# Kernel tuning notes

Hardware: AMD Instinct MI355X
Metric: run time of the kernel (lower is better)

## Reference

```python
import jax, jax.numpy as jnp
import numpy as np

EPS = 1e-5

def _layernorm(x, g, b):
    m = jnp.mean(x, axis=-1, keepdims=True)
    v = jnp.mean((x - m) ** 2, axis=-1, keepdims=True)
    return (x - m) * jax.lax.rsqrt(v + EPS) * g + b

def _mish(x):
    return x * jnp.tanh(jax.nn.softplus(x))

def setup_inputs() -> dict:
    key = jax.random.key(0)
    ks = jax.random.split(key, 6)
    N, D, Hd, P = 768, 256, 256, 128
    return {
        "h_fused": jax.random.normal(ks[0], (N, D), jnp.float32),
        "W0": jax.random.normal(ks[1], (D, Hd), jnp.float32) / np.sqrt(D),
        "b0": jnp.zeros((Hd,), jnp.float32),
        "g0": jnp.ones((Hd,), jnp.float32),
        "be0": jnp.zeros((Hd,), jnp.float32),
        "W1": jax.random.normal(ks[2], (Hd, P), jnp.float32) / np.sqrt(Hd),
        "b1": jnp.zeros((P,), jnp.float32),
        "Wc1": jax.random.normal(ks[3], (2 * P, Hd), jnp.float32) / np.sqrt(2 * P),
        "bc1": jnp.zeros((Hd,), jnp.float32),
        "gc": jnp.ones((Hd,), jnp.float32),
        "bec": jnp.zeros((Hd,), jnp.float32),
        "Wc2": jax.random.normal(ks[4], (Hd, 1), jnp.float32) / np.sqrt(Hd),
        "bc2": jnp.zeros((1,), jnp.float32),
    }

def reference(h_fused, W0, b0, g0, be0, W1, b1, Wc1, bc1, gc, bec, Wc2, bc2):
    # pre_proj: Linear -> LayerNorm -> Mish -> (Dropout p=0) -> Linear
    H = _mish(_layernorm(h_fused @ W0 + b0, g0, be0)) @ W1 + b1  # [N, P]
    P = H.shape[-1]
    # classifier Linear on concat(h_i, h_j): split weight rows so the
    # [N,N,2P] concat tensor is never materialized (identical math).
    Wi, Wj = Wc1[:P], Wc1[P:]
    fi = H @ Wi  # [N, Hd]
    fj = H @ Wj  # [N, Hd]
    pair = fi[:, None, :] + fj[None, :, :] + bc1  # [N, N, Hd]
    h = _mish(_layernorm(pair, gc, bec))
    logits = (h @ Wc2 + bc2)[..., 0]  # [N, N]
    logits = logits[None]  # B=1 (batch_ptr=None path)
    N = logits.shape[-1]
    matrix_mask = jnp.ones((1, N, N), dtype=bool)
    return (logits, matrix_mask)
```

## Files before the change

kernel.cpp:

```cpp
#include <hip/hip_runtime.h>

#define EPS 1e-5f
#define LOGITS_N (768 * 768)
#define LOG2E 1.4426950408889634f
#define LN2   0.6931471805599453f

__device__ __forceinline__ float mishf(float z) {
    float t = __expf(fminf(z, 40.f));
    float u = t * (t + 2.f);
    return z * u * __builtin_amdgcn_rcpf(u + 2.f);
}

__device__ __forceinline__ float block_sum(float v, float* red) {
#pragma unroll
    for (int off = 32; off > 0; off >>= 1) v += __shfl_down(v, off, 64);
    const int lane = threadIdx.x & 63, wid = threadIdx.x >> 6;
    __syncthreads();
    if (lane == 0) red[wid] = v;
    __syncthreads();
    return red[0] + red[1] + red[2] + red[3];
}

__global__ __launch_bounds__(256) void k1_rows(
    const float* __restrict__ h, const float* __restrict__ W0,
    const float* __restrict__ b0, const float* __restrict__ g0,
    const float* __restrict__ be0, const float* __restrict__ W1,
    const float* __restrict__ b1, const float* __restrict__ Wc1,
    const float* __restrict__ bc1, const float* __restrict__ gc,
    const float* __restrict__ bec, const float* __restrict__ wc2,
    float* __restrict__ fi, float* __restrict__ fjb,
    float* __restrict__ stats, float* __restrict__ Gp,
    float* __restrict__ Ep, float* __restrict__ Wp) {
    __shared__ float shi[256][2];
    __shared__ float sai[256][2];
    __shared__ float sHi[128][2];
    __shared__ float red[4];
    __shared__ float part[4][64][12];
    const int t = threadIdx.x;
    const int i0 = blockIdx.x * 2;
    if (blockIdx.x == 0) {
        Gp[t] = gc[t] * LOG2E;
        Ep[t] = bec[t] * LOG2E;
        Wp[t] = wc2[t] * LN2;
    }
    shi[t][0] = h[i0 * 256 + t];
    shi[t][1] = h[i0 * 256 + 256 + t];
    __syncthreads();
    {
        const int kc = t >> 6, jg = t & 63;
        const float* w0p = W0 + (kc * 64) * 256 + jg * 4;
        float ax[2][4] = {};
#pragma unroll 8
        for (int kk = 0; kk < 64; ++kk) {
            float4 w = *(const float4*)(w0p + kk * 256);
            float2 hh = *(const float2*)&shi[kc * 64 + kk][0];
            ax[0][0] = fmaf(hh.x, w.x, ax[0][0]);
            ax[0][1] = fmaf(hh.x, w.y, ax[0][1]);
            ax[0][2] = fmaf(hh.x, w.z, ax[0][2]);
            ax[0][3] = fmaf(hh.x, w.w, ax[0][3]);
            ax[1][0] = fmaf(hh.y, w.x, ax[1][0]);
            ax[1][1] = fmaf(hh.y, w.y, ax[1][1]);
            ax[1][2] = fmaf(hh.y, w.z, ax[1][2]);
            ax[1][3] = fmaf(hh.y, w.w, ax[1][3]);
        }
        float* pp = &part[kc][jg][0];
#pragma unroll
        for (int c = 0; c < 4; ++c) { pp[c * 2] = ax[0][c]; pp[c * 2 + 1] = ax[1][c]; }
    }
    __syncthreads();
    float x0, x1;
    {
        const int m = t >> 2, c = t & 3;
        x0 = b0[t]; x1 = x0;
#pragma unroll
        for (int kc = 0; kc < 4; ++kc) {
            x0 += part[kc][m][c * 2 + 0];
            x1 += part[kc][m][c * 2 + 1];
        }
    }
    {
        float s1 = block_sum(x0, red), s2 = block_sum(x0 * x0, red);
        float mean = s1 * (1.f / 256.f);
        float var = fmaxf(s2 * (1.f / 256.f) - mean * mean, 0.f);
        float rs = __builtin_amdgcn_rsqf(var + EPS);
        sai[t][0] = mishf((x0 - mean) * rs * g0[t] + be0[t]);
        s1 = block_sum(x1, red); s2 = block_sum(x1 * x1, red);
        mean = s1 * (1.f / 256.f);
        var = fmaxf(s2 * (1.f / 256.f) - mean * mean, 0.f);
        rs = __builtin_amdgcn_rsqf(var + EPS);
        sai[t][1] = mishf((x1 - mean) * rs * g0[t] + be0[t]);
    }
    __syncthreads();
    {
        const int kc = t >> 5, jg = t & 31;
        const float* w1p = W1 + (kc * 32) * 128 + jg * 4;
        float ah[2][4] = {};
#pragma unroll 8
        for (int kk = 0; kk < 32; ++kk) {
            float4 w = *(const float4*)(w1p + kk * 128);
            float2 ss = *(const float2*)&sai[kc * 32 + kk][0];
            ah[0][0] = fmaf(ss.x, w.x, ah[0][0]);
            ah[0][1] = fmaf(ss.x, w.y, ah[0][1]);
            ah[0][2] = fmaf(ss.x, w.z, ah[0][2]);
            ah[0][3] = fmaf(ss.x, w.w, ah[0][3]);
            ah[1][0] = fmaf(ss.y, w.x, ah[1][0]);
            ah[1][1] = fmaf(ss.y, w.y, ah[1][1]);
            ah[1][2] = fmaf(ss.y, w.z, ah[1][2]);
            ah[1][3] = fmaf(ss.y, w.w, ah[1][3]);
        }
        float* pp = &part[0][0][0] + (kc * 32 + jg) * 12;
#pragma unroll
        for (int c = 0; c < 4; ++c) { pp[c * 2] = ah[0][c]; pp[c * 2 + 1] = ah[1][c]; }
    }
    __syncthreads();
    {
        const int r = t >> 7, jj = t & 127;
        float hv = b1[jj];
        const float* pf = &part[0][0][0];
#pragma unroll
        for (int kc = 0; kc < 8; ++kc)
            hv += pf[(kc * 32 + (jj >> 2)) * 12 + (jj & 3) * 2 + r];
        sHi[jj][r] = hv;
    }
    __syncthreads();
    float avi[2][4] = {}, avj[2][4] = {};
    {
        const int kc = t >> 6, jg = t & 63;
        const float* wip = Wc1 + (kc * 32) * 256 + jg * 4;
        const float* wjp = Wc1 + (128 + kc * 32) * 256 + jg * 4;
#pragma unroll 4
        for (int kk = 0; kk < 32; ++kk) {
            float4 wa = *(const float4*)(wip + kk * 256);
            float4 wb = *(const float4*)(wjp + kk * 256);
            float2 hh = *(const float2*)&sHi[kc * 32 + kk][0];
            avi[0][0] = fmaf(hh.x, wa.x, avi[0][0]);
            avi[0][1] = fmaf(hh.x, wa.y, avi[0][1]);
            avi[0][2] = fmaf(hh.x, wa.z, avi[0][2]);
            avi[0][3] = fmaf(hh.x, wa.w, avi[0][3]);
            avi[1][0] = fmaf(hh.y, wa.x, avi[1][0]);
            avi[1][1] = fmaf(hh.y, wa.y, avi[1][1]);
            avi[1][2] = fmaf(hh.y, wa.z, avi[1][2]);
            avi[1][3] = fmaf(hh.y, wa.w, avi[1][3]);
            avj[0][0] = fmaf(hh.x, wb.x, avj[0][0]);
            avj[0][1] = fmaf(hh.x, wb.y, avj[0][1]);
            avj[0][2] = fmaf(hh.x, wb.z, avj[0][2]);
            avj[0][3] = fmaf(hh.x, wb.w, avj[0][3]);
            avj[1][0] = fmaf(hh.y, wb.x, avj[1][0]);
            avj[1][1] = fmaf(hh.y, wb.y, avj[1][1]);
            avj[1][2] = fmaf(hh.y, wb.z, avj[1][2]);
            avj[1][3] = fmaf(hh.y, wb.w, avj[1][3]);
        }
        float* pp = &part[kc][jg][0];
#pragma unroll
        for (int c = 0; c < 4; ++c) { pp[c * 2] = avi[0][c]; pp[c * 2 + 1] = avi[1][c]; }
    }
    __syncthreads();
    float vi0 = 0.f, vi1 = 0.f;
    {
        const int m = t >> 2, c = t & 3;
#pragma unroll
        for (int kc = 0; kc < 4; ++kc) {
            vi0 += part[kc][m][c * 2 + 0];
            vi1 += part[kc][m][c * 2 + 1];
        }
    }
    __syncthreads();
    {
        const int kc = t >> 6, jg = t & 63;
        float* pp = &part[kc][jg][0];
#pragma unroll
        for (int c = 0; c < 4; ++c) { pp[c * 2] = avj[0][c]; pp[c * 2 + 1] = avj[1][c]; }
    }
    __syncthreads();
    float vj0, vj1;
    {
        const int m = t >> 2, c = t & 3;
        vj0 = bc1[t]; vj1 = vj0;
#pragma unroll
        for (int kc = 0; kc < 4; ++kc) {
            vj0 += part[kc][m][c * 2 + 0];
            vj1 += part[kc][m][c * 2 + 1];
        }
    }
    fi[i0 * 256 + t] = vi0;
    fi[(i0 + 1) * 256 + t] = vi1;
    fjb[i0 * 256 + t] = vj0;
    fjb[(i0 + 1) * 256 + t] = vj1;
    {
        float su = block_sum(vi0, red), sq = block_sum(vi0 * vi0, red);
        float sv = block_sum(vj0, red), sw = block_sum(vj0 * vj0, red);
        if (t == 0) {
            stats[i0 * 4 + 0] = su * (1.f / 256.f);
            stats[i0 * 4 + 1] = sq * (1.f / 256.f);
            stats[i0 * 4 + 2] = sv * (1.f / 256.f);
            stats[i0 * 4 + 3] = sw * (1.f / 256.f);
        }
        su = block_sum(vi1, red); sq = block_sum(vi1 * vi1, red);
        sv = block_sum(vj1, red); sw = block_sum(vj1 * vj1, red);
        if (t == 0) {
            stats[(i0 + 1) * 4 + 0] = su * (1.f / 256.f);
            stats[(i0 + 1) * 4 + 1] = sq * (1.f / 256.f);
            stats[(i0 + 1) * 4 + 2] = sv * (1.f / 256.f);
            stats[(i0 + 1) * 4 + 3] = sw * (1.f / 256.f);
        }
    }
}

__global__ __launch_bounds__(256) void k3_pair(
    const float* __restrict__ fi, const float* __restrict__ fjb,
    const float* __restrict__ stats, const float* __restrict__ Gp,
    const float* __restrict__ Ep, const float* __restrict__ Wp,
    const float* __restrict__ bc2, float* __restrict__ out, int write_mask) {
    __shared__ float FI[16][260];
    __shared__ float FJ[16][260];
    __shared__ float Gs[256];
    const int tid = threadIdx.x;
    const int i0 = blockIdx.y * 16, j0 = blockIdx.x * 16;
#pragma unroll
    for (int l = 0; l < 4; ++l) {
        int idx = tid + l * 256;
        int r = idx >> 6, c = (idx & 63) * 4;
        *(float4*)&FI[r][c] = *(const float4*)&fi[(i0 + r) * 256 + c];
        *(float4*)&FJ[r][c] = *(const float4*)&fjb[(j0 + r) * 256 + c];
    }
    Gs[tid] = Gp[tid];
    const int ti = tid >> 4, tj = tid & 15;
    float a_i = stats[(i0 + ti) * 4 + 0];
    float s_i = stats[(i0 + ti) * 4 + 1];
    float b_j = stats[(j0 + tj) * 4 + 2];
    float t_j = stats[(j0 + tj) * 4 + 3];
    __syncthreads();
    const float* FIp = &FI[ti][0];
    const float* FJp = &FJ[tj][0];
    float dot[4] = {0.f, 0.f, 0.f, 0.f};
#pragma unroll 8
    for (int d4 = 0; d4 < 64; ++d4) {
        float4 xi = *(const float4*)&FIp[d4 * 4];
        float4 xj = *(const float4*)&FJp[d4 * 4];
        dot[0] = fmaf(xi.x, xj.x, dot[0]);
        dot[1] = fmaf(xi.y, xj.y, dot[1]);
        dot[2] = fmaf(xi.z, xj.z, dot[2]);
        dot[3] = fmaf(xi.w, xj.w, dot[3]);
    }
    float m = a_i + b_j;
    float ex2 = s_i + t_j + (dot[0] + dot[1] + dot[2] + dot[3]) * (2.f / 256.f);
    float var = fmaxf(ex2 - m * m, 0.f);
    float rs = __builtin_amdgcn_rsqf(var + EPS);
    float c0 = -m * rs;
    const float4* Ep4 = (const float4*)Ep;
    const float4* Wp4 = (const float4*)Wp;
    float acc[4] = {0.f, 0.f, 0.f, 0.f};
#pragma unroll 8
    for (int d4 = 0; d4 < 64; ++d4) {
        float4 xi = *(const float4*)&FIp[d4 * 4];
        float4 xj = *(const float4*)&FJp[d4 * 4];
        float4 g4 = *(const float4*)&Gs[d4 * 4];
        float4 e4 = Ep4[d4];
        float4 w4 = Wp4[d4];
        float gs[4] = {g4.x, g4.y, g4.z, g4.w};
        float es[4] = {e4.x, e4.y, e4.z, e4.w};
        float vs[4] = {w4.x, w4.y, w4.z, w4.w};
        float xs[4] = {xi.x + xj.x, xi.y + xj.y, xi.z + xj.z, xi.w + xj.w};
        float y[4], v[4];
#pragma unroll
        for (int c = 0; c < 4; ++c) {
            float p = fmaf(xs[c], rs, c0);
            y[c] = fmaf(p, gs[c], es[c]);
            float tt = __builtin_amdgcn_exp2f(y[c]);
            v[c] = fmaf(tt, tt + 2.f, 2.f);
        }
        float p01 = v[0] * v[1], p23 = v[2] * v[3];
        float rr = __builtin_amdgcn_rcpf(p01 * p23);
        float i01 = rr * p23, i23 = rr * p01;
        float inv[4] = {i01 * v[1], i01 * v[0], i23 * v[3], i23 * v[2]};
#pragma unroll
        for (int c = 0; c < 4; ++c) {
            float my = fmaf(y[c] * inv[c], -2.f, y[c]);
            acc[c] = fmaf(my, vs[c], acc[c]);
        }
    }
    const int oi = (i0 + ti) * 768 + j0 + tj;
    out[oi] = (acc[0] + acc[1]) + (acc[2] + acc[3]) + bc2[0];
    if (write_mask) out[LOGITS_N + oi] = 1.0f;
}

extern "C" void kernel_launch(void* const* d_in, const int* in_sizes, int n_in,
                              void* d_out, int out_size, void* d_ws, size_t ws_size,
                              hipStream_t stream) {
    const float* h   = (const float*)d_in[0];
    const float* W0  = (const float*)d_in[1];
    const float* b0  = (const float*)d_in[2];
    const float* g0  = (const float*)d_in[3];
    const float* be0 = (const float*)d_in[4];
    const float* W1  = (const float*)d_in[5];
    const float* b1  = (const float*)d_in[6];
    const float* Wc1 = (const float*)d_in[7];
    const float* bc1 = (const float*)d_in[8];
    const float* gc  = (const float*)d_in[9];
    const float* bec = (const float*)d_in[10];
    const float* Wc2 = (const float*)d_in[11];
    const float* bc2 = (const float*)d_in[12];
    float* ws = (float*)d_ws;
    float* fi    = ws;
    float* fjb   = ws + 196608;
    float* stats = ws + 393216;
    float* Gp    = ws + 396288;
    float* Ep    = ws + 396544;
    float* Wp    = ws + 396800;
    float* out = (float*)d_out;
    int write_mask = (out_size >= 2 * LOGITS_N) ? 1 : 0;

    k1_rows<<<dim3(384), dim3(256), 0, stream>>>(h, W0, b0, g0, be0, W1, b1,
                                                 Wc1, bc1, gc, bec, Wc2,
                                                 fi, fjb, stats, Gp, Ep, Wp);
    k3_pair<<<dim3(48, 48), dim3(256), 0, stream>>>(fi, fjb, stats, Gp, Ep, Wp,
                                                    bc2, out, write_mask);
}
```

Baseline: 76.49 us.

## Split mish dot into linear part precomputed per row, use packed FP32 math

Mish is rewritten as y - 2y/(t(t+2)+2), so the linear term sum(y*w) is folded into per-row precomputed dot products (Di, Dj) plus the global constants sum(g*w) and sum(e*w) from k1. This leaves only the nonlinear remainder in the pair loop. The pair kernel's inner loops now use v_pk_fma/v_pk_mul/v_pk_add inline asm on float pairs, stage E and W in LDS, and set a launch-bounds occupancy hint of 4. The aim is fewer VALU instructions per element in the dominant N²·Hd loop, at the cost of extra reductions in k1 and a slightly different floating-point summation order.

```diff
diff --git a/kernel.cpp b/kernel.cpp
--- a/kernel.cpp
+++ b/kernel.cpp
@@ -4,6 +4,21 @@
 #define LOGITS_N (768 * 768)
 #define LOG2E 1.4426950408889634f
 #define LN2   0.6931471805599453f
+
+typedef float v2f __attribute__((ext_vector_type(2)));
+typedef float v4f __attribute__((ext_vector_type(4)));
+
+__device__ __forceinline__ v2f pk_add(v2f a, v2f b) {
+    v2f d; asm("v_pk_add_f32 %0, %1, %2" : "=v"(d) : "v"(a), "v"(b)); return d;
+}
+__device__ __forceinline__ v2f pk_mul(v2f a, v2f b) {
+    v2f d; asm("v_pk_mul_f32 %0, %1, %2" : "=v"(d) : "v"(a), "v"(b)); return d;
+}
+__device__ __forceinline__ v2f pk_fma(v2f a, v2f b, v2f c) {
+    v2f d; asm("v_pk_fma_f32 %0, %1, %2, %3" : "=v"(d) : "v"(a), "v"(b), "v"(c)); return d;
+}
+#define LO2(v) __builtin_shufflevector(v, v, 0, 1)
+#define HI2(v) __builtin_shufflevector(v, v, 2, 3)
 
 __device__ __forceinline__ float mishf(float z) {
     float t = __expf(fminf(z, 40.f));
@@ -30,7 +45,8 @@
     const float* __restrict__ bec, const float* __restrict__ wc2,
     float* __restrict__ fi, float* __restrict__ fjb,
     float* __restrict__ stats, float* __restrict__ Gp,
-    float* __restrict__ Ep, float* __restrict__ Wp) {
+    float* __restrict__ Ep, float* __restrict__ Wp,
+    float* __restrict__ consts) {
     __shared__ float shi[256][2];
     __shared__ float sai[256][2];
     __shared__ float sHi[128][2];
@@ -38,10 +54,14 @@
     __shared__ float part[4][64][12];
     const int t = threadIdx.x;
     const int i0 = blockIdx.x * 2;
+    const float u = gc[t] * wc2[t];
     if (blockIdx.x == 0) {
         Gp[t] = gc[t] * LOG2E;
         Ep[t] = bec[t] * LOG2E;
         Wp[t] = wc2[t] * LN2;
+        float sgw = block_sum(u, red);
+        float sew = block_sum(bec[t] * wc2[t], red);
+        if (t == 0) { consts[0] = sgw; consts[1] = sew; }
     }
     shi[t][0] = h[i0 * 256 + t];
     shi[t][1] = h[i0 * 256 + 256 + t];
@@ -189,31 +209,38 @@
     {
         float su = block_sum(vi0, red), sq = block_sum(vi0 * vi0, red);
         float sv = block_sum(vj0, red), sw = block_sum(vj0 * vj0, red);
+        float di = block_sum(vi0 * u, red), dj = block_sum(vj0 * u, red);
         if (t == 0) {
-            stats[i0 * 4 + 0] = su * (1.f / 256.f);
-            stats[i0 * 4 + 1] = sq * (1.f / 256.f);
-            stats[i0 * 4 + 2] = sv * (1.f / 256.f);
-            stats[i0 * 4 + 3] = sw * (1.f / 256.f);
+            stats[i0 * 8 + 0] = su * (1.f / 256.f);
+            stats[i0 * 8 + 1] = sq * (1.f / 256.f);
+            stats[i0 * 8 + 2] = sv * (1.f / 256.f);
+            stats[i0 * 8 + 3] = sw * (1.f / 256.f);
+            stats[i0 * 8 + 4] = di;
+            stats[i0 * 8 + 5] = dj;
         }
         su = block_sum(vi1, red); sq = block_sum(vi1 * vi1, red);
         sv = block_sum(vj1, red); sw = block_sum(vj1 * vj1, red);
+        di = block_sum(vi1 * u, red); dj = block_sum(vj1 * u, red);
         if (t == 0) {
-            stats[(i0 + 1) * 4 + 0] = su * (1.f / 256.f);
-            stats[(i0 + 1) * 4 + 1] = sq * (1.f / 256.f);
-            stats[(i0 + 1) * 4 + 2] = sv * (1.f / 256.f);
-            stats[(i0 + 1) * 4 + 3] = sw * (1.f / 256.f);
-        }
-    }
-}
-
-__global__ __launch_bounds__(256) void k3_pair(
+            stats[(i0 + 1) * 8 + 0] = su * (1.f / 256.f);
+            stats[(i0 + 1) * 8 + 1] = sq * (1.f / 256.f);
+            stats[(i0 + 1) * 8 + 2] = sv * (1.f / 256.f);
+            stats[(i0 + 1) * 8 + 3] = sw * (1.f / 256.f);
+            stats[(i0 + 1) * 8 + 4] = di;
+            stats[(i0 + 1) * 8 + 5] = dj;
+        }
+    }
+}
+
+__global__ __launch_bounds__(256, 4) void k3_pair(
     const float* __restrict__ fi, const float* __restrict__ fjb,
     const float* __restrict__ stats, const float* __restrict__ Gp,
     const float* __restrict__ Ep, const float* __restrict__ Wp,
-    const float* __restrict__ bc2, float* __restrict__ out, int write_mask) {
-    __shared__ float FI[16][260];
-    __shared__ float FJ[16][260];
-    __shared__ float Gs[256];
+    const float* __restrict__ consts, const float* __restrict__ bc2,
+    float* __restrict__ out, int write_mask) {
+    __shared__ __align__(16) float FI[16][260];
+    __shared__ __align__(16) float FJ[16][260];
+    __shared__ __align__(16) float Gs[256], Es[256], Ws[256];
     const int tid = threadIdx.x;
     const int i0 = blockIdx.y * 16, j0 = blockIdx.x * 16;
 #pragma unroll
@@ -224,63 +251,86 @@
         *(float4*)&FJ[r][c] = *(const float4*)&fjb[(j0 + r) * 256 + c];
     }
     Gs[tid] = Gp[tid];
+    Es[tid] = Ep[tid];
+    Ws[tid] = Wp[tid];
     const int ti = tid >> 4, tj = tid & 15;
-    float a_i = stats[(i0 + ti) * 4 + 0];
-    float s_i = stats[(i0 + ti) * 4 + 1];
-    float b_j = stats[(j0 + tj) * 4 + 2];
-    float t_j = stats[(j0 + tj) * 4 + 3];
+    const float mi = stats[(i0 + ti) * 8 + 0];
+    const float qi = stats[(i0 + ti) * 8 + 1];
+    const float Di = stats[(i0 + ti) * 8 + 4];
+    const float mj = stats[(j0 + tj) * 8 + 2];
+    const float qj = stats[(j0 + tj) * 8 + 3];
+    const float Dj = stats[(j0 + tj) * 8 + 5];
+    const float Sgw = consts[0], Sew = consts[1], bc2f = bc2[0];
     __syncthreads();
     const float* FIp = &FI[ti][0];
     const float* FJp = &FJ[tj][0];
-    float dot[4] = {0.f, 0.f, 0.f, 0.f};
+    v2f da = {0.f, 0.f}, db = {0.f, 0.f};
 #pragma unroll 8
-    for (int d4 = 0; d4 < 64; ++d4) {
-        float4 xi = *(const float4*)&FIp[d4 * 4];
-        float4 xj = *(const float4*)&FJp[d4 * 4];
-        dot[0] = fmaf(xi.x, xj.x, dot[0]);
-        dot[1] = fmaf(xi.y, xj.y, dot[1]);
-        dot[2] = fmaf(xi.z, xj.z, dot[2]);
-        dot[3] = fmaf(xi.w, xj.w, dot[3]);
-    }
-    float m = a_i + b_j;
-    float ex2 = s_i + t_j + (dot[0] + dot[1] + dot[2] + dot[3]) * (2.f / 256.f);
-    float var = fmaxf(ex2 - m * m, 0.f);
-    float rs = __builtin_amdgcn_rsqf(var + EPS);
-    float c0 = -m * rs;
-    const float4* Ep4 = (const float4*)Ep;
-    const float4* Wp4 = (const float4*)Wp;
-    float acc[4] = {0.f, 0.f, 0.f, 0.f};
-#pragma unroll 8
-    for (int d4 = 0; d4 < 64; ++d4) {
-        float4 xi = *(const float4*)&FIp[d4 * 4];
-        float4 xj = *(const float4*)&FJp[d4 * 4];
-        float4 g4 = *(const float4*)&Gs[d4 * 4];
-        float4 e4 = Ep4[d4];
-        float4 w4 = Wp4[d4];
-        float gs[4] = {g4.x, g4.y, g4.z, g4.w};
-        float es[4] = {e4.x, e4.y, e4.z, e4.w};
-        float vs[4] = {w4.x, w4.y, w4.z, w4.w};
-        float xs[4] = {xi.x + xj.x, xi.y + xj.y, xi.z + xj.z, xi.w + xj.w};
-        float y[4], v[4];
-#pragma unroll
-        for (int c = 0; c < 4; ++c) {
-            float p = fmaf(xs[c], rs, c0);
-            y[c] = fmaf(p, gs[c], es[c]);
-            float tt = __builtin_amdgcn_exp2f(y[c]);
-            v[c] = fmaf(tt, tt + 2.f, 2.f);
-        }
-        float p01 = v[0] * v[1], p23 = v[2] * v[3];
-        float rr = __builtin_amdgcn_rcpf(p01 * p23);
-        float i01 = rr * p23, i23 = rr * p01;
-        float inv[4] = {i01 * v[1], i01 * v[0], i23 * v[3], i23 * v[2]};
-#pragma unroll
-        for (int c = 0; c < 4; ++c) {
-            float my = fmaf(y[c] * inv[c], -2.f, y[c]);
-            acc[c] = fmaf(my, vs[c], acc[c]);
-        }
-    }
+    for (int d8 = 0; d8 < 32; ++d8) {
+        v4f xiA = *(const v4f*)(FIp + d8 * 8);
+        v4f xiB = *(const v4f*)(FIp + d8 * 8 + 4);
+        v4f xjA = *(const v4f*)(FJp + d8 * 8);
+        v4f xjB = *(const v4f*)(FJp + d8 * 8 + 4);
+        da = pk_fma(LO2(xiA), LO2(xjA), da);
+        db = pk_fma(HI2(xiA), HI2(xjA), db);
+        da = pk_fma(LO2(xiB), LO2(xjB), da);
+        db = pk_fma(HI2(xiB), HI2(xjB), db);
+    }
+    const float dot = (da.x + da.y) + (db.x + db.y);
+    const float m = mi + mj;
+    const float ex2 = qi + qj + dot * (2.f / 256.f);
+    const float var = fmaxf(ex2 - m * m, 0.f);
+    const float rs = __builtin_amdgcn_rsqf(var + EPS);
+    const float c0 = -m * rs;
+    const float lin = fmaf(rs, Di + Dj, fmaf(c0, Sgw, Sew));
+    const v2f rs2 = {rs, rs}, c02 = {c0, c0}, two2 = {2.f, 2.f};
+    v2f accA = {0.f, 0.f}, accB = {0.f, 0.f};
+    const v4f* G4 = (const v4f*)&Gs[0];
+    const v4f* E4 = (const v4f*)&Es[0];
+    const v4f* W4 = (const v4f*)&Ws[0];
+#pragma unroll 2
+    for (int d8 = 0; d8 < 32; ++d8) {
+        v4f xiA = *(const v4f*)(FIp + d8 * 8);
+        v4f xiB = *(const v4f*)(FIp + d8 * 8 + 4);
+        v4f xjA = *(const v4f*)(FJp + d8 * 8);
+        v4f xjB = *(const v4f*)(FJp + d8 * 8 + 4);
+        v4f gA = G4[d8 * 2], gB = G4[d8 * 2 + 1];
+        v4f eA = E4[d8 * 2], eB = E4[d8 * 2 + 1];
+        v4f wA = W4[d8 * 2], wB = W4[d8 * 2 + 1];
+        v2f xs0 = pk_add(LO2(xiA), LO2(xjA));
+        v2f xs1 = pk_add(HI2(xiA), HI2(xjA));
+        v2f xs2 = pk_add(LO2(xiB), LO2(xjB));
+        v2f xs3 = pk_add(HI2(xiB), HI2(xjB));
+        v2f y0 = pk_fma(pk_fma(xs0, rs2, c02), LO2(gA), LO2(eA));
+        v2f y1 = pk_fma(pk_fma(xs1, rs2, c02), HI2(gA), HI2(eA));
+        v2f y2 = pk_fma(pk_fma(xs2, rs2, c02), LO2(gB), LO2(eB));
+        v2f y3 = pk_fma(pk_fma(xs3, rs2, c02), HI2(gB), HI2(eB));
+        v2f t0, t1, t2, t3;
+        t0.x = __builtin_amdgcn_exp2f(y0.x); t0.y = __builtin_amdgcn_exp2f(y0.y);
+        t1.x = __builtin_amdgcn_exp2f(y1.x); t1.y = __builtin_amdgcn_exp2f(y1.y);
+        t2.x = __builtin_amdgcn_exp2f(y2.x); t2.y = __builtin_amdgcn_exp2f(y2.y);
+        t3.x = __builtin_amdgcn_exp2f(y3.x); t3.y = __builtin_amdgcn_exp2f(y3.y);
+        v2f v0 = pk_fma(t0, pk_add(t0, two2), two2);
+        v2f v1 = pk_fma(t1, pk_add(t1, two2), two2);
+        v2f v2_ = pk_fma(t2, pk_add(t2, two2), two2);
+        v2f v3 = pk_fma(t3, pk_add(t3, two2), two2);
+        v2f Pab = pk_mul(v0, v1), Pcd = pk_mul(v2_, v3);
+        v2f Q = pk_mul(Pab, Pcd);
+        float rall = __builtin_amdgcn_rcpf(Q.x * Q.y);
+        v2f R1; R1.x = rall * Q.y; R1.y = rall * Q.x;
+        v2f Rab = pk_mul(R1, Pcd), Rcd = pk_mul(R1, Pab);
+        v2f i0v = pk_mul(Rab, v1);
+        v2f i1v = pk_mul(Rab, v0);
+        v2f i2v = pk_mul(Rcd, v3);
+        v2f i3v = pk_mul(Rcd, v2_);
+        accA = pk_fma(pk_mul(y0, i0v), LO2(wA), accA);
+        accB = pk_fma(pk_mul(y1, i1v), HI2(wA), accB);
+        accA = pk_fma(pk_mul(y2, i2v), LO2(wB), accA);
+        accB = pk_fma(pk_mul(y3, i3v), HI2(wB), accB);
+    }
+    const float nl = (accA.x + accA.y) + (accB.x + accB.y);
     const int oi = (i0 + ti) * 768 + j0 + tj;
-    out[oi] = (acc[0] + acc[1]) + (acc[2] + acc[3]) + bc2[0];
+    out[oi] = fmaf(-2.f, nl, lin) + bc2f;
     if (write_mask) out[LOGITS_N + oi] = 1.0f;
 }
 
@@ -301,18 +351,20 @@
     const float* Wc2 = (const float*)d_in[11];
     const float* bc2 = (const float*)d_in[12];
     float* ws = (float*)d_ws;
-    float* fi    = ws;
-    float* fjb   = ws + 196608;
-    float* stats = ws + 393216;
-    float* Gp    = ws + 396288;
-    float* Ep    = ws + 396544;
-    float* Wp    = ws + 396800;
+    float* fi     = ws;
+    float* fjb    = ws + 196608;
+    float* stats  = ws + 393216;
+    float* Gp     = ws + 399360;
+    float* Ep     = ws + 399616;
+    float* Wp     = ws + 399872;
+    float* consts = ws + 400128;
     float* out = (float*)d_out;
     int write_mask = (out_size >= 2 * LOGITS_N) ? 1 : 0;
 
     k1_rows<<<dim3(384), dim3(256), 0, stream>>>(h, W0, b0, g0, be0, W1, b1,
                                                  Wc1, bc1, gc, bec, Wc2,
-                                                 fi, fjb, stats, Gp, Ep, Wp);
+                                                 fi, fjb, stats, Gp, Ep, Wp,
+                                                 consts);
     k3_pair<<<dim3(48, 48), dim3(256), 0, stream>>>(fi, fjb, stats, Gp, Ep, Wp,
-                                                    bc2, out, write_mask);
-}
+                                                    consts, bc2, out, write_mask);
+}
```

Measured after the change: 68.15 us. 1.12x faster.
